# Kernel optimization log

Measured on AMD Instinct MI355X. Metric: run time of the kernel, lower is better.

Reference implementation:

```python
import jax, jax.numpy as jnp
import numpy as np

NUM_BINS = 10


def setup_inputs() -> dict:
    key = jax.random.key(0)
    k1, k2 = jax.random.split(key)
    N, C = 1_000_000, 128
    logits = jax.random.normal(k1, (N, C), dtype=jnp.float32)
    targets = jax.random.randint(k2, (N,), 0, C, dtype=jnp.int64)
    return {"logits": logits, "targets": targets}


def reference(logits, targets):
    # softmax over classes; confidence = max prob, pred = argmax
    probs = jax.nn.softmax(logits, axis=1)          # [N, C]
    conf = jnp.max(probs, axis=1)                   # [N]
    preds = jnp.argmax(probs, axis=1)               # [N]
    acc = (preds == targets).astype(jnp.float32)    # [N]

    n = conf.shape[0]
    edges = jnp.linspace(0.0, 1.0, NUM_BINS + 1)
    upper = edges[1:]                               # bin i is (edges[i], edges[i+1]]
    # searchsorted(side='left'): first i with upper[i] >= conf -> conf in (low, up]
    bins = jnp.clip(jnp.searchsorted(upper, conf, side="left"), 0, NUM_BINS - 1)

    cnt = jax.ops.segment_sum(jnp.ones_like(conf), bins, num_segments=NUM_BINS)
    conf_sum = jax.ops.segment_sum(conf, bins, num_segments=NUM_BINS)
    acc_sum = jax.ops.segment_sum(acc, bins, num_segments=NUM_BINS)

    nonempty = cnt > 0
    denom = jnp.where(nonempty, cnt, 1.0)
    avg_conf = conf_sum / denom
    avg_acc = acc_sum / denom
    frac = cnt / n                                  # n_inside (mean over all samples)
    ece = jnp.sum(jnp.where(nonempty, jnp.abs(avg_conf - avg_acc) * frac, 0.0))
    return ece.reshape(1)
```

## Files before the change

kernel.cpp:

```cpp
#include <hip/hip_runtime.h>

#define NBINS 10

__global__ void ece_zero_ws(float* __restrict__ ws, const int* __restrict__ t) {
    int i = threadIdx.x;
    if (i < 3 * NBINS) ws[i] = 0.0f;
    if (i == 0) {
        bool is64 = true;
        for (int k = 0; k < 64; ++k) {
            if (t[2 * k + 1] != 0) { is64 = false; break; }
        }
        ws[30] = is64 ? 1.0f : 0.0f;
    }
}

__global__ __launch_bounds__(256) void ece_main(const float* __restrict__ logits,
                                                const int* __restrict__ targets,
                                                float* __restrict__ ws, int n) {
    __shared__ float s_cnt[NBINS], s_conf[NBINS], s_acc[NBINS];
    if (threadIdx.x < NBINS) {
        s_cnt[threadIdx.x] = 0.0f;
        s_conf[threadIdx.x] = 0.0f;
        s_acc[threadIdx.x] = 0.0f;
    }
    const bool t64 = (ws[30] != 0.0f);
    __syncthreads();

    const int lane = threadIdx.x & 63;
    const int half = lane >> 5;
    const int hl   = lane & 31;
    const int wave_in_block   = threadIdx.x >> 6;
    const int waves_per_block = blockDim.x >> 6;
    const long long wave_global =
        (long long)blockIdx.x * waves_per_block + wave_in_block;
    const long long nwaves = (long long)gridDim.x * waves_per_block;
    const long long npairs = ((long long)n + 1) >> 1;

    const float ue[9] = {0.1f, 0.2f, 0.3f, 0.4f, 0.5f, 0.6f, 0.7f, 0.8f, 0.9f};

    for (long long pair = wave_global; pair < npairs; pair += nwaves) {
        const long long row = pair * 2 + half;
        if (row >= n) continue;

        const float4 v =
            *reinterpret_cast<const float4*>(logits + pair * 256 + lane * 4);

        float m = v.x;
        int idx = hl * 4;
        if (v.y > m) { m = v.y; idx = hl * 4 + 1; }
        if (v.z > m) { m = v.z; idx = hl * 4 + 2; }
        if (v.w > m) { m = v.w; idx = hl * 4 + 3; }

        #pragma unroll
        for (int off = 16; off >= 1; off >>= 1) {
            float om = __shfl_xor(m, off, 64);
            int   oi = __shfl_xor(idx, off, 64);
            if (om > m || (om == m && oi < idx)) { m = om; idx = oi; }
        }

        float s = __expf(v.x - m) + __expf(v.y - m) +
                  __expf(v.z - m) + __expf(v.w - m);
        #pragma unroll
        for (int off = 16; off >= 1; off >>= 1)
            s += __shfl_xor(s, off, 64);

        if (hl == 0) {
            float conf = 1.0f / s;
            int bin = 0;
            #pragma unroll
            for (int k = 0; k < 9; ++k) bin += (conf > ue[k]) ? 1 : 0;
            const int tgt = t64 ? targets[2 * row] : targets[row];
            float acc = (idx == tgt) ? 1.0f : 0.0f;
            atomicAdd(&s_cnt[bin], 1.0f);
            atomicAdd(&s_conf[bin], conf);
            atomicAdd(&s_acc[bin], acc);
        }
    }
    __syncthreads();

    if (threadIdx.x < NBINS) {
        atomicAdd(&ws[threadIdx.x],             s_cnt[threadIdx.x]);
        atomicAdd(&ws[NBINS + threadIdx.x],     s_conf[threadIdx.x]);
        atomicAdd(&ws[2 * NBINS + threadIdx.x], s_acc[threadIdx.x]);
    }
}

__global__ void ece_final(const float* __restrict__ ws, float* __restrict__ out,
                          int n) {
    float ece = 0.0f;
    for (int b = 0; b < NBINS; ++b) {
        float cnt = ws[b];
        if (cnt > 0.0f) {
            float avg_conf = ws[NBINS + b] / cnt;
            float avg_acc  = ws[2 * NBINS + b] / cnt;
            float frac = cnt / (float)n;
            ece += fabsf(avg_conf - avg_acc) * frac;
        }
    }
    out[0] = ece;
}

extern "C" void kernel_launch(void* const* d_in, const int* in_sizes, int n_in,
                              void* d_out, int out_size, void* d_ws, size_t ws_size,
                              hipStream_t stream) {
    const float* logits = (const float*)d_in[0];
    const int* targets = (const int*)d_in[1];
    float* ws = (float*)d_ws;
    float* out = (float*)d_out;
    const int n = in_sizes[0] >> 7;

    hipLaunchKernelGGL(ece_zero_ws, dim3(1), dim3(64), 0, stream, ws, targets);

    const int blocks = 2048;
    hipLaunchKernelGGL(ece_main, dim3(blocks), dim3(256), 0, stream,
                       logits, targets, ws, n);

    hipLaunchKernelGGL(ece_final, dim3(1), dim3(1), 0, stream, ws, out, n);
}
```

Measured before the change: 689.8 us.

## Drop zeroing kernel; write per-block partials and reduce in parallel final kernel

Removes the separate workspace-zeroing launch by having each block detect the int64 target layout itself with a wave ballot, and write its bin partials to a private slot instead of global atomics. The final kernel now reduces all block partials with 256 threads and a shared-memory accumulation before computing the ECE. This saves one kernel launch and avoids global atomic contention, at the cost of an extra partials buffer and a slightly heavier final reduction.

```diff
diff --git a/kernel.cpp b/kernel.cpp
--- a/kernel.cpp
+++ b/kernel.cpp
@@ -1,30 +1,25 @@
 #include <hip/hip_runtime.h>
 
 #define NBINS 10
-
-__global__ void ece_zero_ws(float* __restrict__ ws, const int* __restrict__ t) {
-    int i = threadIdx.x;
-    if (i < 3 * NBINS) ws[i] = 0.0f;
-    if (i == 0) {
-        bool is64 = true;
-        for (int k = 0; k < 64; ++k) {
-            if (t[2 * k + 1] != 0) { is64 = false; break; }
-        }
-        ws[30] = is64 ? 1.0f : 0.0f;
-    }
-}
+#define MAIN_BLOCKS 2048
 
 __global__ __launch_bounds__(256) void ece_main(const float* __restrict__ logits,
                                                 const int* __restrict__ targets,
-                                                float* __restrict__ ws, int n) {
+                                                float* __restrict__ part, int n) {
     __shared__ float s_cnt[NBINS], s_conf[NBINS], s_acc[NBINS];
+    __shared__ int s_t64;
     if (threadIdx.x < NBINS) {
         s_cnt[threadIdx.x] = 0.0f;
         s_conf[threadIdx.x] = 0.0f;
         s_acc[threadIdx.x] = 0.0f;
     }
-    const bool t64 = (ws[30] != 0.0f);
+    if ((threadIdx.x >> 6) == 0) {
+        int odd = targets[2 * threadIdx.x + 1];
+        unsigned long long nz = __ballot(odd != 0);
+        if (threadIdx.x == 0) s_t64 = (nz == 0ULL) ? 1 : 0;
+    }
     __syncthreads();
+    const bool t64 = (s_t64 != 0);
 
     const int lane = threadIdx.x & 63;
     const int half = lane >> 5;
@@ -79,25 +74,46 @@
     __syncthreads();
 
     if (threadIdx.x < NBINS) {
-        atomicAdd(&ws[threadIdx.x],             s_cnt[threadIdx.x]);
-        atomicAdd(&ws[NBINS + threadIdx.x],     s_conf[threadIdx.x]);
-        atomicAdd(&ws[2 * NBINS + threadIdx.x], s_acc[threadIdx.x]);
+        float* slot = part + (size_t)blockIdx.x * 32;
+        slot[threadIdx.x]             = s_cnt[threadIdx.x];
+        slot[NBINS + threadIdx.x]     = s_conf[threadIdx.x];
+        slot[2 * NBINS + threadIdx.x] = s_acc[threadIdx.x];
     }
 }
 
-__global__ void ece_final(const float* __restrict__ ws, float* __restrict__ out,
-                          int n) {
-    float ece = 0.0f;
-    for (int b = 0; b < NBINS; ++b) {
-        float cnt = ws[b];
-        if (cnt > 0.0f) {
-            float avg_conf = ws[NBINS + b] / cnt;
-            float avg_acc  = ws[2 * NBINS + b] / cnt;
-            float frac = cnt / (float)n;
-            ece += fabsf(avg_conf - avg_acc) * frac;
+__global__ __launch_bounds__(256) void ece_final(const float* __restrict__ part,
+                                                 float* __restrict__ out,
+                                                 int n, int nblocks) {
+    __shared__ float tot[3 * NBINS];
+    if (threadIdx.x < 3 * NBINS) tot[threadIdx.x] = 0.0f;
+    __syncthreads();
+
+    float loc[3 * NBINS];
+    #pragma unroll
+    for (int k = 0; k < 3 * NBINS; ++k) loc[k] = 0.0f;
+
+    for (int b = threadIdx.x; b < nblocks; b += blockDim.x) {
+        const float* slot = part + (size_t)b * 32;
+        #pragma unroll
+        for (int k = 0; k < 3 * NBINS; ++k) loc[k] += slot[k];
+    }
+    #pragma unroll
+    for (int k = 0; k < 3 * NBINS; ++k) atomicAdd(&tot[k], loc[k]);
+    __syncthreads();
+
+    if (threadIdx.x == 0) {
+        float ece = 0.0f;
+        for (int b = 0; b < NBINS; ++b) {
+            float cnt = tot[b];
+            if (cnt > 0.0f) {
+                float avg_conf = tot[NBINS + b] / cnt;
+                float avg_acc  = tot[2 * NBINS + b] / cnt;
+                float frac = cnt / (float)n;
+                ece += fabsf(avg_conf - avg_acc) * frac;
+            }
         }
+        out[0] = ece;
     }
-    out[0] = ece;
 }
 
 extern "C" void kernel_launch(void* const* d_in, const int* in_sizes, int n_in,
@@ -105,15 +121,12 @@
                               hipStream_t stream) {
     const float* logits = (const float*)d_in[0];
     const int* targets = (const int*)d_in[1];
-    float* ws = (float*)d_ws;
+    float* part = (float*)d_ws;
     float* out = (float*)d_out;
     const int n = in_sizes[0] >> 7;
 
-    hipLaunchKernelGGL(ece_zero_ws, dim3(1), dim3(64), 0, stream, ws, targets);
-
-    const int blocks = 2048;
-    hipLaunchKernelGGL(ece_main, dim3(blocks), dim3(256), 0, stream,
-                       logits, targets, ws, n);
-
-    hipLaunchKernelGGL(ece_final, dim3(1), dim3(1), 0, stream, ws, out, n);
+    hipLaunchKernelGGL(ece_main, dim3(MAIN_BLOCKS), dim3(256), 0, stream,
+                       logits, targets, part, n);
+    hipLaunchKernelGGL(ece_final, dim3(1), dim3(256), 0, stream,
+                       part, out, n, MAIN_BLOCKS);
 }
```

After: 718.0 us. 1.04x slower.
